# Kernel tuning notes

Hardware: AMD Instinct MI355X
Metric: run time of the kernel (lower is better)

## Reference

```python
import jax, jax.numpy as jnp
import numpy as np

RADIUS = 0.1
NSAMPLE = 32


def _ball_query(radius, nsample, xyz, new_xyz):
    # xyz: (B,N,3), new_xyz: (B,npoint,3) -> idx (B,npoint,nsample) int32
    # Faithful to the CUDA ball_query: take the first nsample in-radius indices
    # (in ascending point order); pad with the first found index.
    N = xyz.shape[1]
    d2 = jnp.sum((new_xyz[:, :, None, :] - xyz[:, None, :, :]) ** 2, axis=-1)  # (B,np,N)
    mask = d2 < radius * radius
    key_arr = jnp.where(mask, jnp.arange(N, dtype=jnp.int32), jnp.int32(N))
    idx = jnp.sort(key_arr, axis=-1)[..., :nsample]  # (B,np,ns)
    first = idx[..., :1]
    idx = jnp.where(idx == N, first, idx)
    idx = jnp.where(idx == N, 0, idx)  # empty-ball fallback (matches zero-init buffer)
    return idx


def _group(features, idx):
    # features (B,C,N), idx (B,np,ns) -> (B,C,np,ns)
    return jax.vmap(lambda f, i: f[:, i])(features, idx)


def _forward(xyz, new_xyz):
    idx = jax.lax.stop_gradient(_ball_query(RADIUS, NSAMPLE, xyz, new_xyz))
    xyz_t = jnp.transpose(xyz, (0, 2, 1))                 # (B,3,N)
    g = _group(xyz_t, idx)                                # (B,3,np,ns) grouped_xyz
    c = jnp.transpose(new_xyz, (0, 2, 1))[..., None]      # (B,3,np,1)  new_xyz_reshaped

    # pairwise distances within each group
    diff = g[..., :, None] - g[..., None, :]              # (B,3,np,ns,ns)
    dis = jnp.sqrt(jnp.sum(diff * diff, axis=1))          # (B,np,ns,ns)
    mean_dis = jnp.mean(dis, axis=3)                      # (B,np,ns)
    tip_idx = jnp.argmax(mean_dis, axis=2)                # (B,np)
    tip_pts = jnp.take_along_axis(g, tip_idx[:, None, :, None], axis=3)[..., 0]  # (B,3,np)

    cb = jnp.broadcast_to(c, g.shape)                     # (B,3,np,ns)
    gpv = jnp.cross(jnp.cross(cb, g, axis=1), cb, axis=1)
    gpv = gpv / jnp.linalg.norm(gpv, axis=1)[:, None]     # (B,3,np,ns)

    new_r = jnp.sqrt(jnp.sum(c * c, axis=1))              # (B,np,1)
    new_norm = c / (new_r[:, None] + 1e-8)                # (B,3,np,1)

    c3 = c[..., 0]                                        # (B,3,np)
    tpv = jnp.cross(jnp.cross(c3, tip_pts, axis=1), c3, axis=1)
    tpv = tpv / jnp.linalg.norm(tpv, axis=1)[:, None]     # (B,3,np)

    gcv = jnp.cross(gpv, jnp.broadcast_to(tpv[..., None], gpv.shape), axis=1)
    sinv = jnp.sum(gcv * new_norm, axis=1)                # (B,np,ns)

    dis_t = jnp.transpose(dis, (0, 2, 1, 3))              # (B,ns,np,ns)
    dis_sort = jnp.sort(dis_t, axis=1) * sinv[:, None]    # (B,ns,np,ns)
    grouped_r = jnp.sqrt(jnp.sum(g * g, axis=1))          # (B,np,ns)
    return jnp.concatenate([dis_sort, grouped_r[:, None]], axis=1)  # (B,ns+1,np,ns)


def setup_inputs() -> dict:
    key = jax.random.key(0)
    k1, k2 = jax.random.split(key)
    xyz = jax.random.uniform(k1, (4, 16384, 3), dtype=jnp.float32)
    new_xyz = jax.random.uniform(k2, (4, 2048, 3), dtype=jnp.float32)
    return {"xyz": xyz, "new_xyz": new_xyz}


def reference(xyz, new_xyz):
    return _forward(xyz, new_xyz)
```

## Files before the change

### kernel.cpp

```cpp
#include <hip/hip_runtime.h>


#define BB 4
#define NN 16384
#define MM 2048
#define NS 32
#define R2 0.01f
#define GZ 20
#define NCELL 2000
#define CPAD 2048
#define HCAP 128

#define WS_PTS_OFF (32 * 1024)
#define WS_NEED (WS_PTS_OFF + (size_t)BB * NN * 16)

__device__ __forceinline__ int cell_of(float x, float y, float z) {
    int ci = (int)(x * 10.0f); ci = ci < 0 ? 0 : (ci > 9 ? 9 : ci);
    int cj = (int)(y * 10.0f); cj = cj < 0 ? 0 : (cj > 9 ? 9 : cj);
    int ck = (int)(z * 20.0f); ck = ck < 0 ? 0 : (ck > 19 ? 19 : ck);
    return (ci * 10 + cj) * GZ + ck;
}

__global__ __launch_bounds__(1024) void k_build(const float* __restrict__ xyz,
                                                int* __restrict__ off,
                                                float4* __restrict__ pts) {
    __shared__ int sc[CPAD];
    __shared__ int wsum[16];
    const int b = blockIdx.x, t = threadIdx.x;
    const int lane = t & 63, wid = t >> 6;
    sc[t] = 0; sc[1024 + t] = 0;
    __syncthreads();
    const float* xp = xyz + (size_t)b * NN * 3;
    float X[16], Y[16], Z[16]; int C[16];
    #pragma unroll
    for (int k = 0; k < 16; ++k) {
        int i = k * 1024 + t;
        const float* p = xp + (size_t)i * 3;
        X[k] = p[0]; Y[k] = p[1]; Z[k] = p[2];
        C[k] = cell_of(X[k], Y[k], Z[k]);
        atomicAdd(&sc[C[k]], 1);
    }
    __syncthreads();
    int v0 = sc[2 * t], v1 = sc[2 * t + 1];
    int s = v0 + v1;
    int x = s;
    #pragma unroll
    for (int o = 1; o < 64; o <<= 1) {
        int u = __shfl_up(x, o);
        if (lane >= o) x += u;
    }
    if (lane == 63) wsum[wid] = x;
    __syncthreads();
    int pre = 0;
    #pragma unroll
    for (int i2 = 0; i2 < 16; ++i2) pre += (i2 < wid) ? wsum[i2] : 0;
    int incl = x + pre;
    int excl = incl - s;
    off[b * CPAD + 2 * t] = excl;
    off[b * CPAD + 2 * t + 1] = excl + v0;
    __syncthreads();
    sc[2 * t] = excl; sc[2 * t + 1] = excl + v0;
    __syncthreads();
    #pragma unroll
    for (int k = 0; k < 16; ++k) {
        int pos = atomicAdd(&sc[C[k]], 1);
        int i = k * 1024 + t;
        pts[(size_t)b * NN + pos] = make_float4(X[k], Y[k], Z[k], __int_as_float(i));
    }
}

__global__ __launch_bounds__(256) void qgr_grid_kernel(
    const float* __restrict__ xyz,
    const float* __restrict__ nxyz,
    const int* __restrict__ offi,
    const float4* __restrict__ pts,
    float* __restrict__ out) {

    __shared__ float4 s_hit[4][2][HCAP];
    __shared__ float4 s_sel[4][2][NS];

    const int lane = threadIdx.x & 63;
    const int w = threadIdx.x >> 6;
    const int sub = lane & 31;
    const int half = lane >> 5;
    const int q0 = blockIdx.x * 8 + w * 2;
    const int b = q0 >> 11;

    const float* xb = xyz + (size_t)b * NN * 3;
    const float* nq = nxyz + (size_t)q0 * 3;
    const float cx0 = nq[0], cy0 = nq[1], cz0 = nq[2];
    const float cx1 = nq[3], cy1 = nq[4], cz1 = nq[5];
    const unsigned long long lmask = (1ull << lane) - 1ull;

    const int* offb = offi + b * CPAD;
    const float4* ptsb = pts + (size_t)b * NN;

    int hits01[2];
    for (int tq = 0; tq < 2; ++tq) {
        const float ccx = tq ? cx1 : cx0;
        const float ccy = tq ? cy1 : cy0;
        const float ccz = tq ? cz1 : cz0;

        int ci0 = (int)(ccx * 10.0f); ci0 = ci0 < 0 ? 0 : (ci0 > 9 ? 9 : ci0);
        int cj0 = (int)(ccy * 10.0f); cj0 = cj0 < 0 ? 0 : (cj0 > 9 ? 9 : cj0);
        int ck0 = (int)(ccz * 20.0f); ck0 = ck0 < 0 ? 0 : (ck0 > 19 ? 19 : ck0);
        int zlo = ck0 > 2 ? ck0 - 2 : 0;
        int zhi = ck0 < 17 ? ck0 + 2 : 19;

        int rs[9], rl[9];
        #pragma unroll
        for (int r = 0; r < 9; ++r) { rs[r] = 0; rl[r] = 0; }
        int nr = 0;
        #pragma unroll
        for (int di = -1; di <= 1; ++di) {
            int ii = ci0 + di; if ((unsigned)ii > 9u) continue;
            #pragma unroll
            for (int dj = -1; dj <= 1; ++dj) {
                int jj = cj0 + dj; if ((unsigned)jj > 9u) continue;
                int base2 = (ii * 10 + jj) * GZ;
                int s0 = offb[base2 + zlo];
                int e0 = offb[base2 + zhi + 1];
                int len = e0 - s0;
                if (len > 0) { rs[nr] = s0; rl[nr] = len; ++nr; }
            }
        }

        float4 P[9];
        #pragma unroll
        for (int r = 0; r < 9; ++r) {
            int a = (lane < rl[r]) ? (rs[r] + lane) : 0;
            P[r] = ptsb[a];
        }

        int hits = 0;
        #pragma unroll
        for (int r = 0; r < 9; ++r) {
            float dx = __fsub_rn(ccx, P[r].x);
            float dy = __fsub_rn(ccy, P[r].y);
            float dz = __fsub_rn(ccz, P[r].z);
            float d2 = __fadd_rn(__fadd_rn(__fmul_rn(dx, dx), __fmul_rn(dy, dy)),
                                 __fmul_rn(dz, dz));
            bool hit = (lane < rl[r]) && (d2 < R2);
            unsigned long long bal = __ballot(hit);
            if (bal) {
                int rank = __popcll(bal & lmask);
                int slot = hits + rank;
                if (hit && slot < HCAP) s_hit[w][tq][slot] = P[r];
                hits += __popcll(bal);
            }
        }
        for (int r = 0; r < nr; ++r) {
            for (int t0 = 64; t0 < rl[r]; t0 += 64) {
                int t = t0 + lane;
                bool act = t < rl[r];
                float4 Q = ptsb[rs[r] + (act ? t : 0)];
                float dx = __fsub_rn(ccx, Q.x);
                float dy = __fsub_rn(ccy, Q.y);
                float dz = __fsub_rn(ccz, Q.z);
                float d2 = __fadd_rn(__fadd_rn(__fmul_rn(dx, dx), __fmul_rn(dy, dy)),
                                     __fmul_rn(dz, dz));
                bool hit = act && (d2 < R2);
                unsigned long long bal = __ballot(hit);
                if (bal) {
                    int rank = __popcll(bal & lmask);
                    int slot = hits + rank;
                    if (hit && slot < HCAP) s_hit[w][tq][slot] = Q;
                    hits += __popcll(bal);
                }
            }
        }
        hits01[tq] = hits;
    }

    const int hits = half ? hits01[1] : hits01[0];
    const int cap = hits < HCAP ? hits : HCAP;
    const float ccx = half ? cx1 : cx0;
    const float ccy = half ? cy1 : cy0;
    const float ccz = half ? cz1 : cz0;

    int key[4];
    #pragma unroll
    for (int r = 0; r < 4; ++r) {
        int e = r * 32 + sub;
        int idx_e = __float_as_int(s_hit[w][half][e].w);
        key[r] = (e < cap) ? ((idx_e << 8) | e) : 0x7fffffff;
    }

    #pragma unroll
    for (int k = 2; k <= 16; k <<= 1) {
        #pragma unroll
        for (int j = k >> 1; j > 0; j >>= 1) {
            bool lower = (sub & j) == 0;
            bool asc = (sub & k) == 0;
            bool keepmin = (lower == asc);
            #pragma unroll
            for (int r = 0; r < 4; ++r) {
                int p = __shfl_xor(key[r], j);
                key[r] = keepmin ? min(key[r], p) : max(key[r], p);
            }
        }
    }
    #pragma unroll
    for (int j = 16; j > 0; j >>= 1) {
        bool lower = (sub & j) == 0;
        #pragma unroll
        for (int r = 0; r < 4; ++r) {
            int p = __shfl_xor(key[r], j);
            bool asc = (r & 1) == 0;
            key[r] = (lower == asc) ? min(key[r], p) : max(key[r], p);
        }
    }
    {
        int t0 = min(key[0], key[1]); key[1] = max(key[0], key[1]); key[0] = t0;
        int t2 = max(key[2], key[3]); key[3] = min(key[2], key[3]); key[2] = t2;
    }
    #pragma unroll
    for (int j = 16; j > 0; j >>= 1) {
        bool lower = (sub & j) == 0;
        #pragma unroll
        for (int r = 0; r < 4; ++r) {
            int p = __shfl_xor(key[r], j);
            bool asc = (r & 2) == 0;
            key[r] = (lower == asc) ? min(key[r], p) : max(key[r], p);
        }
    }
    {
        int t0 = min(key[0], key[2]); key[2] = max(key[0], key[2]); key[0] = t0;
        int t1 = min(key[1], key[3]); key[3] = max(key[1], key[3]); key[1] = t1;
        t0 = min(key[0], key[1]); key[1] = max(key[0], key[1]); key[0] = t0;
        t1 = min(key[2], key[3]); key[3] = max(key[2], key[3]); key[2] = t1;
    }
    #pragma unroll
    for (int j = 16; j > 0; j >>= 1) {
        bool lower = (sub & j) == 0;
        #pragma unroll
        for (int r = 0; r < 4; ++r) {
            int p = __shfl_xor(key[r], j);
            key[r] = lower ? min(key[r], p) : max(key[r], p);
        }
    }

    const int found = hits < NS ? hits : NS;
    const int hbase = half << 5;
    float4 sel = make_float4(0.f, 0.f, 0.f, 0.f);
    if (sub < found) sel = s_hit[w][half][key[0] & 0xFF];
    float p0x, p0y, p0z;
    if (found == 0) { p0x = xb[0]; p0y = xb[1]; p0z = xb[2]; }
    else {
        p0x = __shfl(sel.x, hbase); p0y = __shfl(sel.y, hbase); p0z = __shfl(sel.z, hbase);
    }
    if (sub >= found) { sel.x = p0x; sel.y = p0y; sel.z = p0z; }
    const float hx = sel.x, hy = sel.y, hz = sel.z;

    s_sel[w][half][sub] = sel;

    float v[NS];
    #pragma unroll
    for (int ii = 0; ii < NS; ++ii) {
        float4 B = s_sel[w][half][ii];
        float dx = __fsub_rn(B.x, hx);
        float dy = __fsub_rn(B.y, hy);
        float dz = __fsub_rn(B.z, hz);
        v[ii] = sqrtf(__fadd_rn(__fadd_rn(__fmul_rn(dx, dx), __fmul_rn(dy, dy)),
                                __fmul_rn(dz, dz)));
    }

    float r8[8];
    #pragma unroll
    for (int t = 0; t < 8; ++t) {
        r8[t] = __fadd_rn(__fadd_rn(__fadd_rn(v[t], v[t + 8]), v[t + 16]), v[t + 24]);
    }
    float mv = __fadd_rn(__fadd_rn(__fadd_rn(r8[0], r8[1]), __fadd_rn(r8[2], r8[3])),
                         __fadd_rn(__fadd_rn(r8[4], r8[5]), __fadd_rn(r8[6], r8[7])));
    int mi = sub;
    #pragma unroll
    for (int off = 1; off < 32; off <<= 1) {
        float ov = __shfl_xor(mv, off);
        int oi = __shfl_xor(mi, off);
        if (ov > mv || (ov == mv && oi < mi)) { mv = ov; mi = oi; }
    }

    float4 T = s_sel[w][half][mi];
    const float tx = T.x, ty = T.y, tz = T.z;

    float ux = ccy * tz - ccz * ty, uy = ccz * tx - ccx * tz, uz = ccx * ty - ccy * tx;
    float vx = uy * ccz - uz * ccy, vy = uz * ccx - ux * ccz, vz = ux * ccy - uy * ccx;
    float vn = fmaxf(sqrtf(vx * vx + vy * vy + vz * vz), 1e-37f);
    float tnx = vx / vn, tny = vy / vn, tnz = vz / vn;

    float nrm = sqrtf(ccx * ccx + ccy * ccy + ccz * ccz);
    float dn = nrm + 1e-8f;
    float nnx = ccx / dn, nny = ccy / dn, nnz = ccz / dn;

    float ax = ccy * hz - ccz * hy, ay = ccz * hx - ccx * hz, az = ccx * hy - ccy * hx;
    float px = ay * ccz - az * ccy, py = az * ccx - ax * ccz, pz = ax * ccy - ay * ccx;
    float pn = fmaxf(sqrtf(px * px + py * py + pz * pz), 1e-37f);
    px /= pn; py /= pn; pz /= pn;

    float qx = py * tnz - pz * tny;
    float qy = pz * tnx - px * tnz;
    float qz = px * tny - py * tnx;
    float sinv = qx * nnx + qy * nny + qz * nnz;

    float gr = sqrtf(hx * hx + hy * hy + hz * hz);

    const int m_h = (q0 + half) & (MM - 1);
    const size_t rowstride = (size_t)MM * NS;
    const size_t obase = (((size_t)b * 33) * MM + m_h) * NS + sub;
    out[obase + 32 * rowstride] = gr;

    #pragma unroll
    for (int p = 1; p < NS; p <<= 1) {
        #pragma unroll
        for (int k = p; k >= 1; k >>= 1) {
            #pragma unroll
            for (int j = k & (p - 1); j + k < NS; j += 2 * k) {
                #pragma unroll
                for (int i = 0; i < k; ++i) {
                    if (i + j + k < NS) {
                        int x = i + j, y = i + j + k;
                        if ((x / (2 * p)) == (y / (2 * p))) {
                            float lo = fminf(v[x], v[y]);
                            v[y] = fmaxf(v[x], v[y]);
                            v[x] = lo;
                        }
                    }
                }
            }
        }
    }

    #pragma unroll
    for (int ii = 0; ii < NS; ++ii)
        out[obase + (size_t)ii * rowstride] = v[ii] * sinv;
}

#define CHUNKS 4
__global__ __launch_bounds__(256) void qgr_kernel(
    const float* __restrict__ xyz,
    const float* __restrict__ nxyz,
    float* __restrict__ out) {

    __shared__ float s_gx[4][NS], s_gy[4][NS], s_gz[4][NS];
    __shared__ float s_dis[4][NS][NS + 1];

    const int lane = threadIdx.x & 63;
    const int w = threadIdx.x >> 6;
    const int q = blockIdx.x * 4 + w;
    const int b = q >> 11;
    const int m = q & (MM - 1);

    const float* xb = xyz + (size_t)b * NN * 3;
    const float* nq = nxyz + (size_t)q * 3;
    const float cx = nq[0], cy = nq[1], cz = nq[2];
    const unsigned long long lmask = (1ull << lane) - 1ull;

    int cnt = 0;
    for (int base = 0; base < NN; base += 64 * CHUNKS) {
        float X[CHUNKS], Y[CHUNKS], Z[CHUNKS];
        #pragma unroll
        for (int c = 0; c < CHUNKS; ++c) {
            const float* p = xb + (size_t)(base + c * 64 + lane) * 3;
            X[c] = p[0]; Y[c] = p[1]; Z[c] = p[2];
        }
        bool in[CHUNKS];
        #pragma unroll
        for (int c = 0; c < CHUNKS; ++c) {
            float dx = __fsub_rn(cx, X[c]);
            float dy = __fsub_rn(cy, Y[c]);
            float dz = __fsub_rn(cz, Z[c]);
            float d2 = __fadd_rn(__fadd_rn(__fmul_rn(dx, dx), __fmul_rn(dy, dy)),
                                 __fmul_rn(dz, dz));
            in[c] = d2 < R2;
        }
        #pragma unroll
        for (int c = 0; c < CHUNKS; ++c) {
            unsigned long long bal = __ballot(in[c]);
            if (bal) {
                int rank = __popcll(bal & lmask);
                int slot = cnt + rank;
                if (in[c] && slot < NS) {
                    s_gx[w][slot] = X[c]; s_gy[w][slot] = Y[c]; s_gz[w][slot] = Z[c];
                }
                cnt += __popcll(bal);
            }
        }
        if (cnt >= NS) break;
    }
    __syncthreads();

    int found = cnt < NS ? cnt : NS;
    float p0x, p0y, p0z;
    if (found == 0) { p0x = xb[0]; p0y = xb[1]; p0z = xb[2]; }
    else            { p0x = s_gx[w][0]; p0y = s_gy[w][0]; p0z = s_gz[w][0]; }
    if (lane < NS && lane >= found) {
        s_gx[w][lane] = p0x; s_gy[w][lane] = p0y; s_gz[w][lane] = p0z;
    }
    __syncthreads();

    #pragma unroll
    for (int t = 0; t < 16; ++t) {
        int e = t * 64 + lane;
        int di = e >> 5, dj = e & 31;
        float dx = __fsub_rn(s_gx[w][di], s_gx[w][dj]);
        float dy = __fsub_rn(s_gy[w][di], s_gy[w][dj]);
        float dz = __fsub_rn(s_gz[w][di], s_gz[w][dj]);
        s_dis[w][di][dj] =
            sqrtf(__fadd_rn(__fadd_rn(__fmul_rn(dx, dx), __fmul_rn(dy, dy)), __fmul_rn(dz, dz)));
    }
    __syncthreads();

    {
        int i = lane & 31;
        float r[8];
        #pragma unroll
        for (int t = 0; t < 8; ++t) {
            r[t] = __fadd_rn(__fadd_rn(__fadd_rn(s_dis[w][i][t], s_dis[w][i][t + 8]),
                                        s_dis[w][i][t + 16]),
                             s_dis[w][i][t + 24]);
        }
        float mv = __fadd_rn(__fadd_rn(__fadd_rn(r[0], r[1]), __fadd_rn(r[2], r[3])),
                             __fadd_rn(__fadd_rn(r[4], r[5]), __fadd_rn(r[6], r[7])));
        int mi = i;
        #pragma unroll
        for (int off = 1; off < 64; off <<= 1) {
            float ov = __shfl_xor(mv, off);
            int oi = __shfl_xor(mi, off);
            if (ov > mv || (ov == mv && oi < mi)) { mv = ov; mi = oi; }
        }
        float tx = s_gx[w][mi], ty = s_gy[w][mi], tz = s_gz[w][mi];
        float ux = cy * tz - cz * ty, uy = cz * tx - cx * tz, uz = cx * ty - cy * tx;
        float vx = uy * cz - uz * cy, vy = uz * cx - ux * cz, vz = ux * cy - uy * cx;
        float vn = fmaxf(sqrtf(vx * vx + vy * vy + vz * vz), 1e-37f);
        float tnx = vx / vn, tny = vy / vn, tnz = vz / vn;
        float nr = sqrtf(cx * cx + cy * cy + cz * cz);
        float dn = nr + 1e-8f;
        float nnx = cx / dn, nny = cy / dn, nnz = cz / dn;
        int j = lane & 31;
        float gx = s_gx[w][j], gy = s_gy[w][j], gz = s_gz[w][j];
        float ax = cy * gz - cz * gy, ay = cz * gx - cx * gz, az = cx * gy - cy * gx;
        float px = ay * cz - az * cy, py = az * cx - ax * cz, pz = ax * cy - ay * cx;
        float pn = fmaxf(sqrtf(px * px + py * py + pz * pz), 1e-37f);
        px /= pn; py /= pn; pz /= pn;
        float qx = py * tnz - pz * tny;
        float qy = pz * tnx - px * tnz;
        float qz = px * tny - py * tnx;
        float sinv = qx * nnx + qy * nny + qz * nnz;
        float gr = sqrtf(gx * gx + gy * gy + gz * gz);
        const size_t rowstride = (size_t)MM * NS;
        const size_t obase = (((size_t)b * 33) * MM + m) * NS + j;
        if (lane < NS) out[obase + 32 * rowstride] = gr;
        float v[NS];
        #pragma unroll
        for (int ii = 0; ii < NS; ++ii) v[ii] = s_dis[w][ii][j];
        #pragma unroll
        for (int k = 2; k <= NS; k <<= 1) {
            #pragma unroll
            for (int jj = k >> 1; jj > 0; jj >>= 1) {
                #pragma unroll
                for (int ii = 0; ii < NS; ++ii) {
                    int ll = ii ^ jj;
                    if (ll > ii) {
                        bool up = ((ii & k) == 0);
                        float a = v[ii], c2 = v[ll];
                        bool sw = up ? (a > c2) : (a < c2);
                        if (sw) { v[ii] = c2; v[ll] = a; }
                    }
                }
            }
        }
        if (lane < NS) {
            #pragma unroll
            for (int ii = 0; ii < NS; ++ii)
                out[obase + (size_t)ii * rowstride] = v[ii] * sinv;
        }
    }
}

extern "C" void kernel_launch(void* const* d_in, const int* in_sizes, int n_in,
                              void* d_out, int out_size, void* d_ws, size_t ws_size,
                              hipStream_t stream) {
    (void)in_sizes; (void)n_in; (void)out_size;
    const float* xyz = (const float*)d_in[0];
    const float* nxyz = (const float*)d_in[1];
    float* out = (float*)d_out;

    if (d_ws != nullptr && ws_size >= WS_NEED) {
        char* ws = (char*)d_ws;
        int* off = (int*)ws;
        float4* pts = (float4*)(ws + WS_PTS_OFF);
        k_build<<<BB, 1024, 0, stream>>>(xyz, off, pts);
        qgr_grid_kernel<<<(BB * MM) / 8, 256, 0, stream>>>(xyz, nxyz, off, pts, out);
    } else {
        qgr_kernel<<<(BB * MM) / 4, 256, 0, stream>>>(xyz, nxyz, out);
    }
}
```

Before: 103.4 us.

## Split grid build into parallel count, scan and scatter kernels

Replaces the single four-block grid construction kernel with a memset plus three kernels: a fully parallel per-point cell count using global atomics, a per-batch prefix scan, and a parallel scatter of points into cell-sorted order. The old build ran on only four workgroups, leaving most of the GPU idle while it serially processed each batch's points. The new path adds extra launches and contended global atomics, and the order of points within a cell may differ from before.

```diff
diff --git a/kernel.cpp b/kernel.cpp
--- a/kernel.cpp
+++ b/kernel.cpp
@@ -11,7 +11,9 @@
 #define CPAD 2048
 #define HCAP 128
 
-#define WS_PTS_OFF (32 * 1024)
+#define WS_CUR_OFF (32 * 1024)
+#define WS_CNT_OFF (64 * 1024)
+#define WS_PTS_OFF (96 * 1024)
 #define WS_NEED (WS_PTS_OFF + (size_t)BB * NN * 16)
 
 __device__ __forceinline__ int cell_of(float x, float y, float z) {
@@ -21,27 +23,22 @@
     return (ci * 10 + cj) * GZ + ck;
 }
 
-__global__ __launch_bounds__(1024) void k_build(const float* __restrict__ xyz,
-                                                int* __restrict__ off,
-                                                float4* __restrict__ pts) {
-    __shared__ int sc[CPAD];
+__global__ __launch_bounds__(256) void k_count(const float* __restrict__ xyz,
+                                               int* __restrict__ cnt) {
+    int i = blockIdx.x * 256 + threadIdx.x;
+    int b = i >> 14;
+    const float* p = xyz + (size_t)i * 3;
+    atomicAdd(&cnt[b * CPAD + cell_of(p[0], p[1], p[2])], 1);
+}
+
+__global__ __launch_bounds__(1024) void k_scan(const int* __restrict__ cnt,
+                                               int* __restrict__ off,
+                                               int* __restrict__ cur) {
     __shared__ int wsum[16];
     const int b = blockIdx.x, t = threadIdx.x;
     const int lane = t & 63, wid = t >> 6;
-    sc[t] = 0; sc[1024 + t] = 0;
-    __syncthreads();
-    const float* xp = xyz + (size_t)b * NN * 3;
-    float X[16], Y[16], Z[16]; int C[16];
-    #pragma unroll
-    for (int k = 0; k < 16; ++k) {
-        int i = k * 1024 + t;
-        const float* p = xp + (size_t)i * 3;
-        X[k] = p[0]; Y[k] = p[1]; Z[k] = p[2];
-        C[k] = cell_of(X[k], Y[k], Z[k]);
-        atomicAdd(&sc[C[k]], 1);
-    }
-    __syncthreads();
-    int v0 = sc[2 * t], v1 = sc[2 * t + 1];
+    int v0 = cnt[b * CPAD + 2 * t];
+    int v1 = cnt[b * CPAD + 2 * t + 1];
     int s = v0 + v1;
     int x = s;
     #pragma unroll
@@ -58,15 +55,19 @@
     int excl = incl - s;
     off[b * CPAD + 2 * t] = excl;
     off[b * CPAD + 2 * t + 1] = excl + v0;
-    __syncthreads();
-    sc[2 * t] = excl; sc[2 * t + 1] = excl + v0;
-    __syncthreads();
-    #pragma unroll
-    for (int k = 0; k < 16; ++k) {
-        int pos = atomicAdd(&sc[C[k]], 1);
-        int i = k * 1024 + t;
-        pts[(size_t)b * NN + pos] = make_float4(X[k], Y[k], Z[k], __int_as_float(i));
-    }
+    cur[b * CPAD + 2 * t] = excl;
+    cur[b * CPAD + 2 * t + 1] = excl + v0;
+}
+
+__global__ __launch_bounds__(256) void k_scatter(const float* __restrict__ xyz,
+                                                 int* __restrict__ cur,
+                                                 float4* __restrict__ pts) {
+    int i = blockIdx.x * 256 + threadIdx.x;
+    int b = i >> 14;
+    const float* p = xyz + (size_t)i * 3;
+    float x = p[0], y = p[1], z = p[2];
+    int pos = atomicAdd(&cur[b * CPAD + cell_of(x, y, z)], 1);
+    pts[(size_t)b * NN + pos] = make_float4(x, y, z, __int_as_float(i & (NN - 1)));
 }
 
 __global__ __launch_bounds__(256) void qgr_grid_kernel(
@@ -488,8 +489,14 @@
     if (d_ws != nullptr && ws_size >= WS_NEED) {
         char* ws = (char*)d_ws;
         int* off = (int*)ws;
+        int* cur = (int*)(ws + WS_CUR_OFF);
+        int* cnt = (int*)(ws + WS_CNT_OFF);
         float4* pts = (float4*)(ws + WS_PTS_OFF);
-        k_build<<<BB, 1024, 0, stream>>>(xyz, off, pts);
+
+        hipMemsetAsync(cnt, 0, 32 * 1024, stream);
+        k_count<<<(BB * NN) / 256, 256, 0, stream>>>(xyz, cnt);
+        k_scan<<<BB, 1024, 0, stream>>>(cnt, off, cur);
+        k_scatter<<<(BB * NN) / 256, 256, 0, stream>>>(xyz, cur, pts);
         qgr_grid_kernel<<<(BB * MM) / 8, 256, 0, stream>>>(xyz, nxyz, off, pts, out);
     } else {
         qgr_kernel<<<(BB * MM) / 4, 256, 0, stream>>>(xyz, nxyz, out);
```

Result: faster. 98.76 us (-4.5%).
